# Kernel tuning notes

Hardware: AMD Instinct MI355X
Metric: run time of the kernel (lower is better)

Reference implementation:

```python
import jax, jax.numpy as jnp
import numpy as np

EPS = 1e-6
LOG2PI = float(np.log(2.0 * np.pi))


def gauss_lp(x, mu, lv):
    """Diagonal Gaussian log prob. x:[B,D], mu:[K,D], lv:[K,D] -> [B,K]."""
    inv_var = jnp.exp(-lv)                          # [K,D]
    d = x[:, None, :] - mu[None, :, :]              # [B,K,D]
    quad = jnp.sum(d * d * inv_var[None], axis=-1)  # [B,K]
    logdet = jnp.sum(lv, axis=-1)[None]             # [1,K]
    D = mu.shape[-1]
    return -0.5 * (quad + logdet + D * LOG2PI)


def setup_inputs() -> dict:
    key = jax.random.key(0)
    ks = jax.random.split(key, 9)
    T, B, S, A, OBS, CTL = 200, 256, 256, 16, 128, 16
    return {
        "x": jax.random.normal(ks[0], (T, B, OBS), jnp.float32),
        "u": jax.random.normal(ks[1], (T, B, CTL), jnp.float32),
        "obs_mu": jax.random.normal(ks[2], (S, OBS), jnp.float32),
        "obs_lv": 0.1 * jax.random.normal(ks[3], (S, OBS), jnp.float32),
        "ctl_mu": jax.random.normal(ks[4], (A, CTL), jnp.float32),
        "ctl_lv": 0.1 * jax.random.normal(ks[5], (A, CTL), jnp.float32),
        "trans_logits": jax.random.normal(ks[6], (A, S, S), jnp.float32),
        "pi0_logits": jax.random.normal(ks[7], (S,), jnp.float32),
        "act_prior": jax.random.normal(ks[8], (S, A), jnp.float32),
    }


def reference(x, u, obs_mu, obs_lv, ctl_mu, ctl_lv, trans_logits, pi0_logits, act_prior):
    """HMM forward algorithm (ContinuousGaussianHMM._forward).

    Returns:
      alpha_b: [T, B, S] state forward messages
      alpha_a: [T-1, B, A] action forward messages
    """
    S = obs_mu.shape[0]
    trans = jax.nn.softmax(trans_logits, axis=-1)      # [A,S,S]
    log_pi0 = jax.nn.log_softmax(pi0_logits)           # [S]

    # t = 0: initial state prior + observation likelihood
    b0 = jax.nn.softmax(gauss_lp(x[0], obs_mu, obs_lv) + log_pi0[None], axis=-1)  # [B,S]

    def step(b, xu):
        x_t, u_t = xu
        # action prior from belief: softmax(b @ act_prior)
        a_prior = jax.nn.softmax(b @ act_prior, axis=-1)                           # [B,A]
        # ctl_model.infer: posterior over actions given control u_t
        a_t = jax.nn.softmax(gauss_lp(u_t, ctl_mu, ctl_lv) + jnp.log(a_prior + EPS), axis=-1)  # [B,A]
        # action-conditioned transition applied to belief
        m = jnp.einsum('bi,kij->bkj', b, trans)                                    # [B,A,S]
        # original: sum_i(trans*b + eps) => einsum + S*eps
        logp_z = jnp.log(jnp.einsum('bk,bkj->bj', a_t, m) + S * EPS)               # [B,S]
        b_next = jax.nn.softmax(gauss_lp(x_t, obs_mu, obs_lv) + logp_z, axis=-1)   # [B,S]
        return b_next, (b_next, a_t)

    _, (bs, a_s) = jax.lax.scan(step, b0, (x[1:], u[:-1]))
    alpha_b = jnp.concatenate([b0[None], bs], axis=0)   # [T,B,S]
    alpha_a = a_s                                       # [T-1,B,A]
    return alpha_b, alpha_a
```

## Files before the change

kernel.cpp:

```cpp
#include <hip/hip_runtime.h>
#include <hip/hip_bf16.h>
#include <stdint.h>

#define T_STEPS 200
#define BATCH   256
#define NS      256
#define NA      16
#define DOBS    128
#define DCTL    16
#define LOG2PI  1.8378770664093453f
#define EPS_F   1e-6f

typedef float f32x4 __attribute__((ext_vector_type(4)));
typedef short s16x8 __attribute__((ext_vector_type(8)));
typedef short s16x4 __attribute__((ext_vector_type(4)));

static __device__ __forceinline__ unsigned short f2bf(float f) {
    union { float f; unsigned u; } v; v.f = f;
    unsigned u = v.u;
    u += 0x7fffu + ((u >> 16) & 1u);
    return (unsigned short)(u >> 16);
}

static __device__ __forceinline__ void ld4_mall(const float* base,
                                                f32x4& a, f32x4& b, f32x4& c, f32x4& d) {
    asm volatile(
        "global_load_dwordx4 %0, %4, off offset:0 sc0 sc1\n\t"
        "global_load_dwordx4 %1, %4, off offset:1024 sc0 sc1\n\t"
        "global_load_dwordx4 %2, %4, off offset:2048 sc0 sc1\n\t"
        "global_load_dwordx4 %3, %4, off offset:3072 sc0 sc1\n\t"
        "s_waitcnt vmcnt(0)"
        : "=&v"(a), "=&v"(b), "=&v"(c), "=&v"(d)
        : "v"(base)
        : "memory");
}
static __device__ __forceinline__ void st_mall(float* p, f32x4 v) {
    asm volatile("global_store_dwordx4 %0, %1, off sc0 sc1" :: "v"(p), "v"(v) : "memory");
}

__global__ __launch_bounds__(128) void k_prep_obs(const float* __restrict__ obs_mu,
                                                  const float* __restrict__ obs_lv,
                                                  float* __restrict__ WT,
                                                  float* __restrict__ Cs) {
    int s = blockIdx.x, d = threadIdx.x;
    float lv = obs_lv[s * DOBS + d];
    float mu = obs_mu[s * DOBS + d];
    float iv = expf(-lv);
    WT[d * NS + s]          = -0.5f * iv;
    WT[(DOBS + d) * NS + s] = mu * iv;
    float part = mu * mu * iv + lv;
    for (int m = 1; m < 64; m <<= 1) part += __shfl_xor(part, m, 64);
    __shared__ float red[2];
    if ((threadIdx.x & 63) == 0) red[threadIdx.x >> 6] = part;
    __syncthreads();
    if (threadIdx.x == 0) Cs[s] = -0.5f * (red[0] + red[1] + DOBS * LOG2PI);
}

__global__ __launch_bounds__(256) void k_prep_ctl(const float* __restrict__ cmu,
                                                  const float* __restrict__ clv,
                                                  float* __restrict__ cw1,
                                                  float* __restrict__ cw2,
                                                  float* __restrict__ cc) {
    int t = threadIdx.x;
    int a = t >> 4, d = t & 15;
    float lv = clv[a * DCTL + d];
    float mu = cmu[a * DCTL + d];
    float iv = expf(-lv);
    cw1[t] = -0.5f * iv;
    cw2[t] = mu * iv;
    float part = mu * mu * iv + lv;
    for (int m = 1; m < 16; m <<= 1) part += __shfl_xor(part, m, 64);
    if (d == 0) cc[a] = -0.5f * (part + DCTL * LOG2PI);
}

__global__ __launch_bounds__(64) void k_prep_pi0(const float* __restrict__ pl,
                                                 float* __restrict__ lpi0) {
    int l = threadIdx.x;
    float v[4]; float m = -1e30f;
    for (int k = 0; k < 4; k++) { v[k] = pl[l + 64 * k]; m = fmaxf(m, v[k]); }
    for (int mm = 1; mm < 64; mm <<= 1) m = fmaxf(m, __shfl_xor(m, mm, 64));
    float ssum = 0.f;
    for (int k = 0; k < 4; k++) ssum += expf(v[k] - m);
    for (int mm = 1; mm < 64; mm <<= 1) ssum += __shfl_xor(ssum, mm, 64);
    float ls = logf(ssum);
    for (int k = 0; k < 4; k++) lpi0[l + 64 * k] = v[k] - m - ls;
}

__global__ __launch_bounds__(256) void k_init(float* __restrict__ lg) {
    int idx = blockIdx.x * 256 + threadIdx.x;
    float nv = __int_as_float(0x7FC00000);
    f32x4 n4 = {nv, nv, nv, nv};
    st_mall(lg + (size_t)idx * 4, n4);
}

__global__ __launch_bounds__(256) void k_trans(const float* __restrict__ tl,
                                               __hip_bfloat16* __restrict__ TRf) {
    int wave = threadIdx.x >> 6, lane = threadIdx.x & 63;
    int row = blockIdx.x * 4 + wave;
    int a = row >> 8, i = row & 255;
    const float* src = tl + (size_t)row * NS;
    float v[4]; float m = -1e30f;
    for (int k = 0; k < 4; k++) { v[k] = src[lane + 64 * k]; m = fmaxf(m, v[k]); }
    for (int mm = 1; mm < 64; mm <<= 1) m = fmaxf(m, __shfl_xor(m, mm, 64));
    float ssum = 0.f; float ev[4];
    for (int k = 0; k < 4; k++) { ev[k] = expf(v[k] - m); ssum += ev[k]; }
    for (int mm = 1; mm < 64; mm <<= 1) ssum += __shfl_xor(ssum, mm, 64);
    float inv = 1.f / ssum;
    int kk = i >> 5;
    int lsub = ((i >> 3) & 3) * 16 + a;
    int e = i & 7;
    for (int k = 0; k < 4; k++) {
        int j = lane + 64 * k;
        float p = ev[k] * inv;
        TRf[((size_t)(j * 8 + kk) * 64 + lsub) * 8 + e] = __float2bfloat16(p);
    }
}

__global__ __launch_bounds__(64) void k_prep_ap(const float* __restrict__ ap,
                                                __hip_bfloat16* __restrict__ APh,
                                                __hip_bfloat16* __restrict__ APl) {
    int kk = blockIdx.x, lane = threadIdx.x;
    for (int e = 0; e < 8; e++) {
        int i = kk * 32 + (lane >> 4) * 8 + e;
        int a = lane & 15;
        float v = ap[i * NA + a];
        __hip_bfloat16 hb = __float2bfloat16(v);
        float hi = __bfloat162float(hb);
        APh[(kk * 64 + lane) * 8 + e] = hb;
        APl[(kk * 64 + lane) * 8 + e] = __float2bfloat16(v - hi);
    }
}

__global__ __launch_bounds__(256) void k_obslp(const float* __restrict__ x,
                                               const float* __restrict__ WT,
                                               const float* __restrict__ Cs,
                                               float* __restrict__ obs) {
    __shared__ float f[32 * 256];
    int r0 = blockIdx.x * 32;
    for (int idx = threadIdx.x; idx < 32 * DOBS; idx += 256) {
        int r = idx >> 7, d = idx & 127;
        float v = x[(size_t)(r0 + r) * DOBS + d];
        f[r * 256 + d] = v * v;
        f[r * 256 + 128 + d] = v;
    }
    __syncthreads();
    int s = threadIdx.x;
    float acc[32];
#pragma unroll
    for (int r = 0; r < 32; r++) acc[r] = 0.f;
    for (int d4 = 0; d4 < 64; d4++) {
        float w0 = WT[(d4 * 4 + 0) * NS + s];
        float w1 = WT[(d4 * 4 + 1) * NS + s];
        float w2 = WT[(d4 * 4 + 2) * NS + s];
        float w3 = WT[(d4 * 4 + 3) * NS + s];
#pragma unroll
        for (int r = 0; r < 32; r++) {
            f32x4 fv = *reinterpret_cast<const f32x4*>(&f[r * 256 + d4 * 4]);
            acc[r] += fv.x * w0 + fv.y * w1 + fv.z * w2 + fv.w * w3;
        }
    }
    float c = Cs[s];
#pragma unroll
    for (int r = 0; r < 32; r++) obs[(size_t)(r0 + r) * NS + s] = acc[r] + c;
}

__global__ __launch_bounds__(256) void k_ctllp(const float* __restrict__ u,
                                               const float* __restrict__ cw1,
                                               const float* __restrict__ cw2,
                                               const float* __restrict__ cc,
                                               float* __restrict__ ctl) {
    int idx = blockIdx.x * 256 + threadIdx.x;
    int r = idx >> 4, a = idx & 15;
    const float* ur = u + (size_t)r * DCTL;
    const float* w1 = cw1 + a * DCTL;
    const float* w2 = cw2 + a * DCTL;
    float acc = cc[a];
#pragma unroll
    for (int d = 0; d < 16; d++) {
        float uv = ur[d];
        acc += uv * uv * w1[d] + uv * w2[d];
    }
    ctl[idx] = acc;
}

struct ScanArgs {
    const float* obs;
    const float* ctlp;
    const float* lpi0;
    const __hip_bfloat16* TRf;
    const __hip_bfloat16* APh;
    const __hip_bfloat16* APl;
    float* lg;
    float* out_ab;
    float* out_aa;
};

__global__ __launch_bounds__(256, 1) void k_scan_p(ScanArgs A) {
    const int bid  = blockIdx.x;
    const int bt   = bid >> 4;
    const int jt   = bid & 15;
    const int tid  = threadIdx.x;
    const int wv   = tid >> 6, lane = tid & 63;
    const int kgrp = lane >> 4, arow = lane & 15;
    const int b0   = bt * 16;

    __shared__ __align__(16) char PLb[16 * 512];
    __shared__ float out_t[16][16];

    const float nv = __int_as_float(0x7FC00000);
    const f32x4 n4 = {nv, nv, nv, nv};

    s16x8 bfr[4][8];
#pragma unroll
    for (int q = 0; q < 4; q++) {
        int ct = jt * 16 + wv * 4 + q;
#pragma unroll
        for (int kk = 0; kk < 8; kk++)
            bfr[q][kk] = *((const s16x8*)A.TRf + (size_t)(ct * 8 + kk) * 64 + lane);
    }
    s16x8 aph[8], apl[8];
#pragma unroll
    for (int kk = 0; kk < 8; kk++) {
        aph[kk] = *((const s16x8*)A.APh + kk * 64 + lane);
        apl[kk] = *((const s16x8*)A.APl + kk * 64 + lane);
    }
    f32x4 lp0 = *(const f32x4*)&A.lpi0[lane * 4];

    const float* obs_pf_p = A.obs + ((size_t)BATCH + b0 + kgrp * 4) * NS + jt * 16 + wv * 4;
    const float* ctl_p    = A.ctlp + ((size_t)b0 + kgrp * 4) * NA + arow;
    float*       ab_p     = A.out_ab + ((size_t)b0 + wv * 4) * NS + lane * 4;
    float*       aa_p     = A.out_aa + ((size_t)b0 + kgrp * 4) * NA + arow;
    const float* obs0_p   = A.obs + (size_t)(b0 + wv * 4) * NS + lane * 4;
    const float* lg_ld    = A.lg + ((size_t)b0 + wv * 4) * NS + lane * 4;
    float*       lg_st    = A.lg + ((size_t)b0 + (lane >> 2)) * NS + jt * 16 + (lane & 3) * 4;

    for (int s = 0; s < T_STEPS - 1; s++) {
        f32x4 obs_pfv[4];
#pragma unroll
        for (int r = 0; r < 4; r++)
            obs_pfv[r] = *(const f32x4*)&obs_pf_p[r * NS];
        float ctl_pf[4];
#pragma unroll
        for (int q = 0; q < 4; q++)
            ctl_pf[q] = ctl_p[q * NA];

        f32x4 V[4];
        if (s == 0) {
#pragma unroll
            for (int q = 0; q < 4; q++) {
                f32x4 o = *(const f32x4*)&obs0_p[q * NS];
                V[q] = o + lp0;
            }
        } else {
            const float* rb = lg_ld + ((size_t)(s & 3) << 16);
            for (;;) {
                ld4_mall(rb, V[0], V[1], V[2], V[3]);
                float chk = ((V[0].x + V[0].y) + (V[0].z + V[0].w))
                          + ((V[1].x + V[1].y) + (V[1].z + V[1].w))
                          + ((V[2].x + V[2].y) + (V[2].z + V[2].w))
                          + ((V[3].x + V[3].y) + (V[3].z + V[3].w));
                if (chk == chk) break;
            }
        }

        if (s >= 2 && wv == 0)
            st_mall(lg_st + ((size_t)((s + 2) & 3) << 16), n4);

#pragma unroll
        for (int q = 0; q < 4; q++) {
            int r = wv * 4 + q;
            float m = fmaxf(fmaxf(V[q].x, V[q].y), fmaxf(V[q].z, V[q].w));
            for (int mm = 1; mm < 64; mm <<= 1) m = fmaxf(m, __shfl_xor(m, mm, 64));
            float e0 = __expf(V[q].x - m), e1 = __expf(V[q].y - m);
            float e2 = __expf(V[q].z - m), e3 = __expf(V[q].w - m);
            float ss = (e0 + e1) + (e2 + e3);
            for (int mm = 1; mm < 64; mm <<= 1) ss += __shfl_xor(ss, mm, 64);
            float inv = 1.f / ss;
            float p0 = e0 * inv, p1 = e1 * inv, p2 = e2 * inv, p3 = e3 * inv;
            if ((lane >> 2) == jt) {
                f32x4 pv = {p0, p1, p2, p3};
                *(f32x4*)&ab_p[q * NS] = pv;
            }
            s16x4 sv;
            sv[0] = (short)f2bf(p0); sv[1] = (short)f2bf(p1);
            sv[2] = (short)f2bf(p2); sv[3] = (short)f2bf(p3);
            *(s16x4*)(PLb + r * 512 + ((lane * 8) ^ ((r & 7) << 4))) = sv;
        }
        __syncthreads();

        s16x8 afr[8];
        {
            int sw = (arow & 7) << 4;
#pragma unroll
            for (int kk = 0; kk < 8; kk++)
                afr[kk] = *(const s16x8*)(PLb + arow * 512 + ((kk * 64 + kgrp * 16) ^ sw));
        }

        f32x4 gh = {0.f, 0.f, 0.f, 0.f}, gl = {0.f, 0.f, 0.f, 0.f};
#pragma unroll
        for (int kk = 0; kk < 8; kk++) {
            gh = __builtin_amdgcn_mfma_f32_16x16x32_bf16(afr[kk], aph[kk], gh, 0, 0, 0);
            gl = __builtin_amdgcn_mfma_f32_16x16x32_bf16(afr[kk], apl[kk], gl, 0, 0, 0);
        }
        float at[4];
#pragma unroll
        for (int q = 0; q < 4; q++) {
            float gv = gh[q] + gl[q];
            float m = gv;
            for (int mm = 1; mm < 16; mm <<= 1) m = fmaxf(m, __shfl_xor(m, mm, 64));
            float e1 = __expf(gv - m);
            float s1 = e1;
            for (int mm = 1; mm < 16; mm <<= 1) s1 += __shfl_xor(s1, mm, 64);
            float apr = e1 / s1;
            float al = ctl_pf[q] + __logf(apr + EPS_F);
            float m2 = al;
            for (int mm = 1; mm < 16; mm <<= 1) m2 = fmaxf(m2, __shfl_xor(m2, mm, 64));
            float e2 = __expf(al - m2);
            float s2 = e2;
            for (int mm = 1; mm < 16; mm <<= 1) s2 += __shfl_xor(s2, mm, 64);
            at[q] = e2 / s2;
            if (jt == 0)
                aa_p[q * NA] = at[q];
        }

#pragma unroll
        for (int q2 = 0; q2 < 4; q2++) {
            f32x4 acc = {0.f, 0.f, 0.f, 0.f};
#pragma unroll
            for (int kk = 0; kk < 8; kk++)
                acc = __builtin_amdgcn_mfma_f32_16x16x32_bf16(afr[kk], bfr[q2][kk], acc, 0, 0, 0);
#pragma unroll
            for (int r = 0; r < 4; r++) {
                float vv = acc[r] * at[r];
                for (int mm = 1; mm < 16; mm <<= 1) vv += __shfl_xor(vv, mm, 64);
                if (arow == 0)
                    out_t[kgrp * 4 + r][wv * 4 + q2] =
                        obs_pfv[r][q2] + __logf(vv + NS * EPS_F);
            }
        }
        __syncthreads();

        if (wv == 0) {
            f32x4 val = *(const f32x4*)&out_t[lane >> 2][(lane & 3) * 4];
            st_mall(lg_st + ((size_t)((s + 1) & 3) << 16), val);
        }
        obs_pf_p += (size_t)BATCH * NS;
        ctl_p    += (size_t)BATCH * NA;
        ab_p     += (size_t)BATCH * NS;
        aa_p     += (size_t)BATCH * NA;
    }

    f32x4 V[4];
    {
        const float* rb = lg_ld + ((size_t)((T_STEPS - 1) & 3) << 16);
        for (;;) {
            ld4_mall(rb, V[0], V[1], V[2], V[3]);
            float chk = ((V[0].x + V[0].y) + (V[0].z + V[0].w))
                      + ((V[1].x + V[1].y) + (V[1].z + V[1].w))
                      + ((V[2].x + V[2].y) + (V[2].z + V[2].w))
                      + ((V[3].x + V[3].y) + (V[3].z + V[3].w));
            if (chk == chk) break;
        }
    }
#pragma unroll
    for (int q = 0; q < 4; q++) {
        float m = fmaxf(fmaxf(V[q].x, V[q].y), fmaxf(V[q].z, V[q].w));
        for (int mm = 1; mm < 64; mm <<= 1) m = fmaxf(m, __shfl_xor(m, mm, 64));
        float e0 = __expf(V[q].x - m), e1 = __expf(V[q].y - m);
        float e2 = __expf(V[q].z - m), e3 = __expf(V[q].w - m);
        float ss = (e0 + e1) + (e2 + e3);
        for (int mm = 1; mm < 64; mm <<= 1) ss += __shfl_xor(ss, mm, 64);
        float inv = 1.f / ss;
        if ((lane >> 2) == jt) {
            f32x4 pv = {e0 * inv, e1 * inv, e2 * inv, e3 * inv};
            *(f32x4*)&ab_p[q * NS] = pv;
        }
    }
}

extern "C" void kernel_launch(void* const* d_in, const int* in_sizes, int n_in,
                              void* d_out, int out_size, void* d_ws, size_t ws_size,
                              hipStream_t stream) {
    const float* x            = (const float*)d_in[0];
    const float* u            = (const float*)d_in[1];
    const float* obs_mu       = (const float*)d_in[2];
    const float* obs_lv       = (const float*)d_in[3];
    const float* ctl_mu       = (const float*)d_in[4];
    const float* ctl_lv       = (const float*)d_in[5];
    const float* trans_logits = (const float*)d_in[6];
    const float* pi0_logits   = (const float*)d_in[7];
    const float* act_prior    = (const float*)d_in[8];

    float* out_ab = (float*)d_out;
    float* out_aa = out_ab + (size_t)T_STEPS * BATCH * NS;

    char* w = (char*)d_ws;
    size_t off = 0;
    auto alloc = [&](size_t bytes) -> void* {
        void* pp = w + off;
        off += (bytes + 255) & ~(size_t)255;
        return pp;
    };
    float* WT   = (float*)alloc((size_t)256 * 256 * 4);
    float* Cs   = (float*)alloc(256 * 4);
    float* cw1  = (float*)alloc(256 * 4);
    float* cw2  = (float*)alloc(256 * 4);
    float* cc   = (float*)alloc(16 * 4);
    float* lpi0 = (float*)alloc(256 * 4);
    __hip_bfloat16* TRf = (__hip_bfloat16*)alloc((size_t)4096 * 256 * 2);
    __hip_bfloat16* APh = (__hip_bfloat16*)alloc((size_t)8 * 64 * 8 * 2);
    __hip_bfloat16* APl = (__hip_bfloat16*)alloc((size_t)8 * 64 * 8 * 2);
    float* obs  = (float*)alloc((size_t)T_STEPS * BATCH * NS * 4);
    float* ctlp = (float*)alloc((size_t)(T_STEPS - 1) * BATCH * NA * 4);
    float* lg   = (float*)alloc((size_t)4 * BATCH * NS * 4);
    if (off > ws_size) return;

    k_init<<<256, 256, 0, stream>>>(lg);
    k_prep_obs<<<256, 128, 0, stream>>>(obs_mu, obs_lv, WT, Cs);
    k_prep_ctl<<<1, 256, 0, stream>>>(ctl_mu, ctl_lv, cw1, cw2, cc);
    k_prep_pi0<<<1, 64, 0, stream>>>(pi0_logits, lpi0);
    k_trans<<<1024, 256, 0, stream>>>(trans_logits, TRf);
    k_prep_ap<<<8, 64, 0, stream>>>(act_prior, APh, APl);
    k_obslp<<<1600, 256, 0, stream>>>(x, WT, Cs, obs);
    k_ctllp<<<3184, 256, 0, stream>>>(u, cw1, cw2, cc, ctlp);

    ScanArgs args;
    args.obs = obs; args.ctlp = ctlp; args.lpi0 = lpi0;
    args.TRf = TRf; args.APh = APh; args.APl = APl;
    args.lg = lg;
    args.out_ab = out_ab; args.out_aa = out_aa;
    k_scan_p<<<256, 256, 0, stream>>>(args);
}
```

Measured before the change: 2.087 ms.

## Fuse observation and control log-likelihood computation into the persistent scan kernel

Removes the separate k_obslp and k_ctllp precompute kernels and their large intermediate buffers. Each scan block now loads x and u per step, computes the Gaussian log-likelihoods for its 16 rows and 16 states/actions from weights staged in LDS, and uses them directly. This cuts the global write and read of the obs/ctl tensors and two launches. In exchange it adds per-step compute and an extra LDS pass on the sequential critical path. The step-0 initial belief is also computed in-kernel.

```diff
diff --git a/kernel.cpp b/kernel.cpp
--- a/kernel.cpp
+++ b/kernel.cpp
@@ -131,61 +131,14 @@
     }
 }
 
-__global__ __launch_bounds__(256) void k_obslp(const float* __restrict__ x,
-                                               const float* __restrict__ WT,
-                                               const float* __restrict__ Cs,
-                                               float* __restrict__ obs) {
-    __shared__ float f[32 * 256];
-    int r0 = blockIdx.x * 32;
-    for (int idx = threadIdx.x; idx < 32 * DOBS; idx += 256) {
-        int r = idx >> 7, d = idx & 127;
-        float v = x[(size_t)(r0 + r) * DOBS + d];
-        f[r * 256 + d] = v * v;
-        f[r * 256 + 128 + d] = v;
-    }
-    __syncthreads();
-    int s = threadIdx.x;
-    float acc[32];
-#pragma unroll
-    for (int r = 0; r < 32; r++) acc[r] = 0.f;
-    for (int d4 = 0; d4 < 64; d4++) {
-        float w0 = WT[(d4 * 4 + 0) * NS + s];
-        float w1 = WT[(d4 * 4 + 1) * NS + s];
-        float w2 = WT[(d4 * 4 + 2) * NS + s];
-        float w3 = WT[(d4 * 4 + 3) * NS + s];
-#pragma unroll
-        for (int r = 0; r < 32; r++) {
-            f32x4 fv = *reinterpret_cast<const f32x4*>(&f[r * 256 + d4 * 4]);
-            acc[r] += fv.x * w0 + fv.y * w1 + fv.z * w2 + fv.w * w3;
-        }
-    }
-    float c = Cs[s];
-#pragma unroll
-    for (int r = 0; r < 32; r++) obs[(size_t)(r0 + r) * NS + s] = acc[r] + c;
-}
-
-__global__ __launch_bounds__(256) void k_ctllp(const float* __restrict__ u,
-                                               const float* __restrict__ cw1,
-                                               const float* __restrict__ cw2,
-                                               const float* __restrict__ cc,
-                                               float* __restrict__ ctl) {
-    int idx = blockIdx.x * 256 + threadIdx.x;
-    int r = idx >> 4, a = idx & 15;
-    const float* ur = u + (size_t)r * DCTL;
-    const float* w1 = cw1 + a * DCTL;
-    const float* w2 = cw2 + a * DCTL;
-    float acc = cc[a];
-#pragma unroll
-    for (int d = 0; d < 16; d++) {
-        float uv = ur[d];
-        acc += uv * uv * w1[d] + uv * w2[d];
-    }
-    ctl[idx] = acc;
-}
-
 struct ScanArgs {
-    const float* obs;
-    const float* ctlp;
+    const float* x;
+    const float* u;
+    const float* WT;
+    const float* Cs;
+    const float* cw1;
+    const float* cw2;
+    const float* cc;
     const float* lpi0;
     const __hip_bfloat16* TRf;
     const __hip_bfloat16* APh;
@@ -203,9 +156,17 @@
     const int wv   = tid >> 6, lane = tid & 63;
     const int kgrp = lane >> 4, arow = lane & 15;
     const int b0   = bt * 16;
+    const int dr   = tid >> 4, dc = tid & 15;
 
     __shared__ __align__(16) char PLb[16 * 512];
     __shared__ float out_t[16][16];
+    __shared__ __align__(16) float fL[16][132];
+    __shared__ float uL[16][20];
+    __shared__ __align__(16) float W1L[16][132];
+    __shared__ __align__(16) float W2L[16][132];
+    __shared__ float cw1L[16][20], cw2L[16][20];
+    __shared__ float obsL[16][16];
+    __shared__ float ctlL[16][16];
 
     const float nv = __int_as_float(0x7FC00000);
     const f32x4 n4 = {nv, nv, nv, nv};
@@ -224,34 +185,85 @@
         aph[kk] = *((const s16x8*)A.APh + kk * 64 + lane);
         apl[kk] = *((const s16x8*)A.APl + kk * 64 + lane);
     }
-    f32x4 lp0 = *(const f32x4*)&A.lpi0[lane * 4];
-
-    const float* obs_pf_p = A.obs + ((size_t)BATCH + b0 + kgrp * 4) * NS + jt * 16 + wv * 4;
-    const float* ctl_p    = A.ctlp + ((size_t)b0 + kgrp * 4) * NA + arow;
-    float*       ab_p     = A.out_ab + ((size_t)b0 + wv * 4) * NS + lane * 4;
-    float*       aa_p     = A.out_aa + ((size_t)b0 + kgrp * 4) * NA + arow;
-    const float* obs0_p   = A.obs + (size_t)(b0 + wv * 4) * NS + lane * 4;
-    const float* lg_ld    = A.lg + ((size_t)b0 + wv * 4) * NS + lane * 4;
-    float*       lg_st    = A.lg + ((size_t)b0 + (lane >> 2)) * NS + jt * 16 + (lane & 3) * 4;
+
+    {
+        int dbase = dr * 8;
+#pragma unroll
+        for (int k = 0; k < 8; k++) {
+            W1L[dc][dbase + k] = A.WT[(size_t)(dbase + k) * NS + jt * 16 + dc];
+            W2L[dc][dbase + k] = A.WT[(size_t)(128 + dbase + k) * NS + jt * 16 + dc];
+        }
+        cw1L[dc][dr] = A.cw1[dc * DCTL + dr];
+        cw2L[dc][dr] = A.cw2[dc * DCTL + dr];
+    }
+    const float csv = A.Cs[jt * 16 + dc];
+    const float ccv = A.cc[dc];
+    const float lpv = A.lpi0[jt * 16 + dc];
+    __syncthreads();
+
+    float*       ab_p  = A.out_ab + ((size_t)b0 + wv * 4) * NS + lane * 4;
+    float*       aa_p  = A.out_aa + ((size_t)b0 + kgrp * 4) * NA + arow;
+    const float* lg_ld = A.lg + ((size_t)b0 + wv * 4) * NS + lane * 4;
+    float*       lg_st = A.lg + ((size_t)b0 + (lane >> 2)) * NS + jt * 16 + (lane & 3) * 4;
+    const float* x_p   = A.x + ((size_t)b0 + dr) * DOBS + dc * 8;
+    const float* u_p   = A.u + ((size_t)b0 + dr) * DCTL + dc;
+
+    {
+        f32x4 xa = *(const f32x4*)&x_p[0];
+        f32x4 xb = *(const f32x4*)&x_p[4];
+        *(f32x4*)&fL[dr][dc * 8]     = xa;
+        *(f32x4*)&fL[dr][dc * 8 + 4] = xb;
+        float acc = csv;
+#pragma unroll
+        for (int k = 0; k < 32; k++) {
+            f32x4 xv = *(const f32x4*)&fL[dr][k * 4];
+            f32x4 w1 = *(const f32x4*)&W1L[dc][k * 4];
+            f32x4 w2 = *(const f32x4*)&W2L[dc][k * 4];
+            acc += xv.x * xv.x * w1.x + xv.x * w2.x;
+            acc += xv.y * xv.y * w1.y + xv.y * w2.y;
+            acc += xv.z * xv.z * w1.z + xv.z * w2.z;
+            acc += xv.w * xv.w * w1.w + xv.w * w2.w;
+        }
+        out_t[dr][dc] = acc + lpv;
+        __syncthreads();
+        if (wv == 0) {
+            f32x4 val = *(const f32x4*)&out_t[lane >> 2][(lane & 3) * 4];
+            st_mall(lg_st, val);
+        }
+        x_p += (size_t)BATCH * DOBS;
+    }
 
     for (int s = 0; s < T_STEPS - 1; s++) {
-        f32x4 obs_pfv[4];
-#pragma unroll
-        for (int r = 0; r < 4; r++)
-            obs_pfv[r] = *(const f32x4*)&obs_pf_p[r * NS];
-        float ctl_pf[4];
-#pragma unroll
-        for (int q = 0; q < 4; q++)
-            ctl_pf[q] = ctl_p[q * NA];
+        {
+            f32x4 xa = *(const f32x4*)&x_p[0];
+            f32x4 xb = *(const f32x4*)&x_p[4];
+            float uv1 = u_p[0];
+            *(f32x4*)&fL[dr][dc * 8]     = xa;
+            *(f32x4*)&fL[dr][dc * 8 + 4] = xb;
+            uL[dr][dc] = uv1;
+            float acc = csv;
+#pragma unroll
+            for (int k = 0; k < 32; k++) {
+                f32x4 xv = *(const f32x4*)&fL[dr][k * 4];
+                f32x4 w1 = *(const f32x4*)&W1L[dc][k * 4];
+                f32x4 w2 = *(const f32x4*)&W2L[dc][k * 4];
+                acc += xv.x * xv.x * w1.x + xv.x * w2.x;
+                acc += xv.y * xv.y * w1.y + xv.y * w2.y;
+                acc += xv.z * xv.z * w1.z + xv.z * w2.z;
+                acc += xv.w * xv.w * w1.w + xv.w * w2.w;
+            }
+            obsL[dr][dc] = acc;
+            float ca = ccv;
+#pragma unroll
+            for (int d = 0; d < 16; d++) {
+                float uv = uL[dr][d];
+                ca += uv * uv * cw1L[dc][d] + uv * cw2L[dc][d];
+            }
+            ctlL[dr][dc] = ca;
+        }
 
         f32x4 V[4];
-        if (s == 0) {
-#pragma unroll
-            for (int q = 0; q < 4; q++) {
-                f32x4 o = *(const f32x4*)&obs0_p[q * NS];
-                V[q] = o + lp0;
-            }
-        } else {
+        {
             const float* rb = lg_ld + ((size_t)(s & 3) << 16);
             for (;;) {
                 ld4_mall(rb, V[0], V[1], V[2], V[3]);
@@ -312,7 +324,7 @@
             float s1 = e1;
             for (int mm = 1; mm < 16; mm <<= 1) s1 += __shfl_xor(s1, mm, 64);
             float apr = e1 / s1;
-            float al = ctl_pf[q] + __logf(apr + EPS_F);
+            float al = ctlL[kgrp * 4 + q][arow] + __logf(apr + EPS_F);
             float m2 = al;
             for (int mm = 1; mm < 16; mm <<= 1) m2 = fmaxf(m2, __shfl_xor(m2, mm, 64));
             float e2 = __expf(al - m2);
@@ -335,7 +347,7 @@
                 for (int mm = 1; mm < 16; mm <<= 1) vv += __shfl_xor(vv, mm, 64);
                 if (arow == 0)
                     out_t[kgrp * 4 + r][wv * 4 + q2] =
-                        obs_pfv[r][q2] + __logf(vv + NS * EPS_F);
+                        obsL[kgrp * 4 + r][wv * 4 + q2] + __logf(vv + NS * EPS_F);
             }
         }
         __syncthreads();
@@ -344,10 +356,10 @@
             f32x4 val = *(const f32x4*)&out_t[lane >> 2][(lane & 3) * 4];
             st_mall(lg_st + ((size_t)((s + 1) & 3) << 16), val);
         }
-        obs_pf_p += (size_t)BATCH * NS;
-        ctl_p    += (size_t)BATCH * NA;
-        ab_p     += (size_t)BATCH * NS;
-        aa_p     += (size_t)BATCH * NA;
+        x_p  += (size_t)BATCH * DOBS;
+        u_p  += (size_t)BATCH * DCTL;
+        ab_p += (size_t)BATCH * NS;
+        aa_p += (size_t)BATCH * NA;
     }
 
     f32x4 V[4];
@@ -410,8 +422,6 @@
     __hip_bfloat16* TRf = (__hip_bfloat16*)alloc((size_t)4096 * 256 * 2);
     __hip_bfloat16* APh = (__hip_bfloat16*)alloc((size_t)8 * 64 * 8 * 2);
     __hip_bfloat16* APl = (__hip_bfloat16*)alloc((size_t)8 * 64 * 8 * 2);
-    float* obs  = (float*)alloc((size_t)T_STEPS * BATCH * NS * 4);
-    float* ctlp = (float*)alloc((size_t)(T_STEPS - 1) * BATCH * NA * 4);
     float* lg   = (float*)alloc((size_t)4 * BATCH * NS * 4);
     if (off > ws_size) return;
 
@@ -421,11 +431,12 @@
     k_prep_pi0<<<1, 64, 0, stream>>>(pi0_logits, lpi0);
     k_trans<<<1024, 256, 0, stream>>>(trans_logits, TRf);
     k_prep_ap<<<8, 64, 0, stream>>>(act_prior, APh, APl);
-    k_obslp<<<1600, 256, 0, stream>>>(x, WT, Cs, obs);
-    k_ctllp<<<3184, 256, 0, stream>>>(u, cw1, cw2, cc, ctlp);
 
     ScanArgs args;
-    args.obs = obs; args.ctlp = ctlp; args.lpi0 = lpi0;
+    args.x = x; args.u = u;
+    args.WT = WT; args.Cs = Cs;
+    args.cw1 = cw1; args.cw2 = cw2; args.cc = cc;
+    args.lpi0 = lpi0;
     args.TRf = TRf; args.APh = APh; args.APl = APl;
     args.lg = lg;
     args.out_ab = out_ab; args.out_aa = out_aa;
```

Result: slower. 2.219 ms (+6.3%).

## Interleave two batch tiles per block to hide cross-block scan latency

Applied to the files above, without the earlier changes.

Each block now handles two batch tiles (bt and bt+8) and alternates their scan steps, with half as many blocks launched. While one tile waits on the cross-block exchange of log-messages through the global ring buffer, the block does useful work on the other tile, so the polling latency of the dependent recurrence is hidden. In exchange each block does twice the serial work per step and uses half the CUs, which adds compute time per step.

```diff
diff --git a/kernel.cpp b/kernel.cpp
--- a/kernel.cpp
+++ b/kernel.cpp
@@ -195,164 +195,143 @@
     float* out_aa;
 };
 
-__global__ __launch_bounds__(256, 1) void k_scan_p(ScanArgs A) {
-    const int bid  = blockIdx.x;
-    const int bt   = bid >> 4;
-    const int jt   = bid & 15;
-    const int tid  = threadIdx.x;
-    const int wv   = tid >> 6, lane = tid & 63;
-    const int kgrp = lane >> 4, arow = lane & 15;
-    const int b0   = bt * 16;
-
-    __shared__ __align__(16) char PLb[16 * 512];
-    __shared__ float out_t[16][16];
-
-    const float nv = __int_as_float(0x7FC00000);
-    const f32x4 n4 = {nv, nv, nv, nv};
-
-    s16x8 bfr[4][8];
+struct Ctx {
+    const float* obs_pf;
+    const float* ctl_p;
+    float*       ab_p;
+    float*       aa_p;
+    const float* obs0_p;
+    const float* lg_ld;
+    float*       lg_st;
+};
+
+static __device__ __forceinline__ void scan_phase(
+    int s, int jt, int lane, int wv, int kgrp, int arow, Ctx& C,
+    const s16x8 (&bfr)[4][8], const s16x8 (&aph)[8], const s16x8 (&apl)[8],
+    const f32x4& lp0, const f32x4& n4,
+    char* PLb, float (*out_t)[16])
+{
+    f32x4 obs_pfv[4];
+#pragma unroll
+    for (int r = 0; r < 4; r++)
+        obs_pfv[r] = *(const f32x4*)&C.obs_pf[r * NS];
+    float ctl_pf[4];
+#pragma unroll
+    for (int q = 0; q < 4; q++)
+        ctl_pf[q] = C.ctl_p[q * NA];
+
+    f32x4 V[4];
+    if (s == 0) {
+#pragma unroll
+        for (int q = 0; q < 4; q++) {
+            f32x4 o = *(const f32x4*)&C.obs0_p[q * NS];
+            V[q] = o + lp0;
+        }
+    } else {
+        const float* rb = C.lg_ld + ((size_t)(s & 3) << 16);
+        for (;;) {
+            ld4_mall(rb, V[0], V[1], V[2], V[3]);
+            float chk = ((V[0].x + V[0].y) + (V[0].z + V[0].w))
+                      + ((V[1].x + V[1].y) + (V[1].z + V[1].w))
+                      + ((V[2].x + V[2].y) + (V[2].z + V[2].w))
+                      + ((V[3].x + V[3].y) + (V[3].z + V[3].w));
+            if (chk == chk) break;
+        }
+    }
+
+    if (s >= 2 && wv == 0)
+        st_mall(C.lg_st + ((size_t)((s + 2) & 3) << 16), n4);
+
 #pragma unroll
     for (int q = 0; q < 4; q++) {
-        int ct = jt * 16 + wv * 4 + q;
+        int r = wv * 4 + q;
+        float m = fmaxf(fmaxf(V[q].x, V[q].y), fmaxf(V[q].z, V[q].w));
+        for (int mm = 1; mm < 64; mm <<= 1) m = fmaxf(m, __shfl_xor(m, mm, 64));
+        float e0 = __expf(V[q].x - m), e1 = __expf(V[q].y - m);
+        float e2 = __expf(V[q].z - m), e3 = __expf(V[q].w - m);
+        float ss = (e0 + e1) + (e2 + e3);
+        for (int mm = 1; mm < 64; mm <<= 1) ss += __shfl_xor(ss, mm, 64);
+        float inv = 1.f / ss;
+        float p0 = e0 * inv, p1 = e1 * inv, p2 = e2 * inv, p3 = e3 * inv;
+        if ((lane >> 2) == jt) {
+            f32x4 pv = {p0, p1, p2, p3};
+            *(f32x4*)&C.ab_p[q * NS] = pv;
+        }
+        s16x4 sv;
+        sv[0] = (short)f2bf(p0); sv[1] = (short)f2bf(p1);
+        sv[2] = (short)f2bf(p2); sv[3] = (short)f2bf(p3);
+        *(s16x4*)(PLb + r * 512 + ((lane * 8) ^ ((r & 7) << 4))) = sv;
+    }
+    __syncthreads();
+
+    s16x8 afr[8];
+    {
+        int sw = (arow & 7) << 4;
 #pragma unroll
         for (int kk = 0; kk < 8; kk++)
-            bfr[q][kk] = *((const s16x8*)A.TRf + (size_t)(ct * 8 + kk) * 64 + lane);
-    }
-    s16x8 aph[8], apl[8];
+            afr[kk] = *(const s16x8*)(PLb + arow * 512 + ((kk * 64 + kgrp * 16) ^ sw));
+    }
+
+    f32x4 gh = {0.f, 0.f, 0.f, 0.f}, gl = {0.f, 0.f, 0.f, 0.f};
 #pragma unroll
     for (int kk = 0; kk < 8; kk++) {
-        aph[kk] = *((const s16x8*)A.APh + kk * 64 + lane);
-        apl[kk] = *((const s16x8*)A.APl + kk * 64 + lane);
-    }
-    f32x4 lp0 = *(const f32x4*)&A.lpi0[lane * 4];
-
-    const float* obs_pf_p = A.obs + ((size_t)BATCH + b0 + kgrp * 4) * NS + jt * 16 + wv * 4;
-    const float* ctl_p    = A.ctlp + ((size_t)b0 + kgrp * 4) * NA + arow;
-    float*       ab_p     = A.out_ab + ((size_t)b0 + wv * 4) * NS + lane * 4;
-    float*       aa_p     = A.out_aa + ((size_t)b0 + kgrp * 4) * NA + arow;
-    const float* obs0_p   = A.obs + (size_t)(b0 + wv * 4) * NS + lane * 4;
-    const float* lg_ld    = A.lg + ((size_t)b0 + wv * 4) * NS + lane * 4;
-    float*       lg_st    = A.lg + ((size_t)b0 + (lane >> 2)) * NS + jt * 16 + (lane & 3) * 4;
-
-    for (int s = 0; s < T_STEPS - 1; s++) {
-        f32x4 obs_pfv[4];
-#pragma unroll
-        for (int r = 0; r < 4; r++)
-            obs_pfv[r] = *(const f32x4*)&obs_pf_p[r * NS];
-        float ctl_pf[4];
-#pragma unroll
-        for (int q = 0; q < 4; q++)
-            ctl_pf[q] = ctl_p[q * NA];
-
-        f32x4 V[4];
-        if (s == 0) {
-#pragma unroll
-            for (int q = 0; q < 4; q++) {
-                f32x4 o = *(const f32x4*)&obs0_p[q * NS];
-                V[q] = o + lp0;
-            }
-        } else {
-            const float* rb = lg_ld + ((size_t)(s & 3) << 16);
-            for (;;) {
-                ld4_mall(rb, V[0], V[1], V[2], V[3]);
-                float chk = ((V[0].x + V[0].y) + (V[0].z + V[0].w))
-                          + ((V[1].x + V[1].y) + (V[1].z + V[1].w))
-                          + ((V[2].x + V[2].y) + (V[2].z + V[2].w))
-                          + ((V[3].x + V[3].y) + (V[3].z + V[3].w));
-                if (chk == chk) break;
-            }
-        }
-
-        if (s >= 2 && wv == 0)
-            st_mall(lg_st + ((size_t)((s + 2) & 3) << 16), n4);
-
-#pragma unroll
-        for (int q = 0; q < 4; q++) {
-            int r = wv * 4 + q;
-            float m = fmaxf(fmaxf(V[q].x, V[q].y), fmaxf(V[q].z, V[q].w));
-            for (int mm = 1; mm < 64; mm <<= 1) m = fmaxf(m, __shfl_xor(m, mm, 64));
-            float e0 = __expf(V[q].x - m), e1 = __expf(V[q].y - m);
-            float e2 = __expf(V[q].z - m), e3 = __expf(V[q].w - m);
-            float ss = (e0 + e1) + (e2 + e3);
-            for (int mm = 1; mm < 64; mm <<= 1) ss += __shfl_xor(ss, mm, 64);
-            float inv = 1.f / ss;
-            float p0 = e0 * inv, p1 = e1 * inv, p2 = e2 * inv, p3 = e3 * inv;
-            if ((lane >> 2) == jt) {
-                f32x4 pv = {p0, p1, p2, p3};
-                *(f32x4*)&ab_p[q * NS] = pv;
-            }
-            s16x4 sv;
-            sv[0] = (short)f2bf(p0); sv[1] = (short)f2bf(p1);
-            sv[2] = (short)f2bf(p2); sv[3] = (short)f2bf(p3);
-            *(s16x4*)(PLb + r * 512 + ((lane * 8) ^ ((r & 7) << 4))) = sv;
-        }
-        __syncthreads();
-
-        s16x8 afr[8];
-        {
-            int sw = (arow & 7) << 4;
-#pragma unroll
-            for (int kk = 0; kk < 8; kk++)
-                afr[kk] = *(const s16x8*)(PLb + arow * 512 + ((kk * 64 + kgrp * 16) ^ sw));
-        }
-
-        f32x4 gh = {0.f, 0.f, 0.f, 0.f}, gl = {0.f, 0.f, 0.f, 0.f};
-#pragma unroll
-        for (int kk = 0; kk < 8; kk++) {
-            gh = __builtin_amdgcn_mfma_f32_16x16x32_bf16(afr[kk], aph[kk], gh, 0, 0, 0);
-            gl = __builtin_amdgcn_mfma_f32_16x16x32_bf16(afr[kk], apl[kk], gl, 0, 0, 0);
-        }
-        float at[4];
-#pragma unroll
-        for (int q = 0; q < 4; q++) {
-            float gv = gh[q] + gl[q];
-            float m = gv;
-            for (int mm = 1; mm < 16; mm <<= 1) m = fmaxf(m, __shfl_xor(m, mm, 64));
-            float e1 = __expf(gv - m);
-            float s1 = e1;
-            for (int mm = 1; mm < 16; mm <<= 1) s1 += __shfl_xor(s1, mm, 64);
-            float apr = e1 / s1;
-            float al = ctl_pf[q] + __logf(apr + EPS_F);
-            float m2 = al;
-            for (int mm = 1; mm < 16; mm <<= 1) m2 = fmaxf(m2, __shfl_xor(m2, mm, 64));
-            float e2 = __expf(al - m2);
-            float s2 = e2;
-            for (int mm = 1; mm < 16; mm <<= 1) s2 += __shfl_xor(s2, mm, 64);
-            at[q] = e2 / s2;
-            if (jt == 0)
-                aa_p[q * NA] = at[q];
-        }
-
-#pragma unroll
-        for (int q2 = 0; q2 < 4; q2++) {
-            f32x4 acc = {0.f, 0.f, 0.f, 0.f};
-#pragma unroll
-            for (int kk = 0; kk < 8; kk++)
-                acc = __builtin_amdgcn_mfma_f32_16x16x32_bf16(afr[kk], bfr[q2][kk], acc, 0, 0, 0);
-#pragma unroll
-            for (int r = 0; r < 4; r++) {
-                float vv = acc[r] * at[r];
-                for (int mm = 1; mm < 16; mm <<= 1) vv += __shfl_xor(vv, mm, 64);
-                if (arow == 0)
-                    out_t[kgrp * 4 + r][wv * 4 + q2] =
-                        obs_pfv[r][q2] + __logf(vv + NS * EPS_F);
-            }
-        }
-        __syncthreads();
-
-        if (wv == 0) {
-            f32x4 val = *(const f32x4*)&out_t[lane >> 2][(lane & 3) * 4];
-            st_mall(lg_st + ((size_t)((s + 1) & 3) << 16), val);
-        }
-        obs_pf_p += (size_t)BATCH * NS;
-        ctl_p    += (size_t)BATCH * NA;
-        ab_p     += (size_t)BATCH * NS;
-        aa_p     += (size_t)BATCH * NA;
-    }
-
+        gh = __builtin_amdgcn_mfma_f32_16x16x32_bf16(afr[kk], aph[kk], gh, 0, 0, 0);
+        gl = __builtin_amdgcn_mfma_f32_16x16x32_bf16(afr[kk], apl[kk], gl, 0, 0, 0);
+    }
+    float at[4];
+#pragma unroll
+    for (int q = 0; q < 4; q++) {
+        float gv = gh[q] + gl[q];
+        float m = gv;
+        for (int mm = 1; mm < 16; mm <<= 1) m = fmaxf(m, __shfl_xor(m, mm, 64));
+        float e1 = __expf(gv - m);
+        float s1 = e1;
+        for (int mm = 1; mm < 16; mm <<= 1) s1 += __shfl_xor(s1, mm, 64);
+        float apr = e1 / s1;
+        float al = ctl_pf[q] + __logf(apr + EPS_F);
+        float m2 = al;
+        for (int mm = 1; mm < 16; mm <<= 1) m2 = fmaxf(m2, __shfl_xor(m2, mm, 64));
+        float e2 = __expf(al - m2);
+        float s2 = e2;
+        for (int mm = 1; mm < 16; mm <<= 1) s2 += __shfl_xor(s2, mm, 64);
+        at[q] = e2 / s2;
+        if (jt == 0)
+            C.aa_p[q * NA] = at[q];
+    }
+
+#pragma unroll
+    for (int q2 = 0; q2 < 4; q2++) {
+        f32x4 acc = {0.f, 0.f, 0.f, 0.f};
+#pragma unroll
+        for (int kk = 0; kk < 8; kk++)
+            acc = __builtin_amdgcn_mfma_f32_16x16x32_bf16(afr[kk], bfr[q2][kk], acc, 0, 0, 0);
+#pragma unroll
+        for (int r = 0; r < 4; r++) {
+            float vv = acc[r] * at[r];
+            for (int mm = 1; mm < 16; mm <<= 1) vv += __shfl_xor(vv, mm, 64);
+            if (arow == 0)
+                out_t[kgrp * 4 + r][wv * 4 + q2] =
+                    obs_pfv[r][q2] + __logf(vv + NS * EPS_F);
+        }
+    }
+    __syncthreads();
+
+    if (wv == 0) {
+        f32x4 val = *(const f32x4*)&out_t[lane >> 2][(lane & 3) * 4];
+        st_mall(C.lg_st + ((size_t)((s + 1) & 3) << 16), val);
+    }
+    C.obs_pf += (size_t)BATCH * NS;
+    C.ctl_p  += (size_t)BATCH * NA;
+    C.ab_p   += (size_t)BATCH * NS;
+    C.aa_p   += (size_t)BATCH * NA;
+}
+
+static __device__ __forceinline__ void final_softmax(
+    int jt, int lane, const Ctx& C)
+{
     f32x4 V[4];
     {
-        const float* rb = lg_ld + ((size_t)((T_STEPS - 1) & 3) << 16);
+        const float* rb = C.lg_ld + ((size_t)((T_STEPS - 1) & 3) << 16);
         for (;;) {
             ld4_mall(rb, V[0], V[1], V[2], V[3]);
             float chk = ((V[0].x + V[0].y) + (V[0].z + V[0].w))
@@ -373,9 +352,64 @@
         float inv = 1.f / ss;
         if ((lane >> 2) == jt) {
             f32x4 pv = {e0 * inv, e1 * inv, e2 * inv, e3 * inv};
-            *(f32x4*)&ab_p[q * NS] = pv;
-        }
-    }
+            *(f32x4*)&C.ab_p[q * NS] = pv;
+        }
+    }
+}
+
+__global__ __launch_bounds__(256, 1) void k_scan_p(ScanArgs A) {
+    const int bid  = blockIdx.x;
+    const int btA  = bid >> 4;
+    const int btB  = btA + 8;
+    const int jt   = bid & 15;
+    const int tid  = threadIdx.x;
+    const int wv   = tid >> 6, lane = tid & 63;
+    const int kgrp = lane >> 4, arow = lane & 15;
+
+    __shared__ __align__(16) char PLb[16 * 512];
+    __shared__ float out_t[16][16];
+
+    const float nv = __int_as_float(0x7FC00000);
+    const f32x4 n4 = {nv, nv, nv, nv};
+
+    s16x8 bfr[4][8];
+#pragma unroll
+    for (int q = 0; q < 4; q++) {
+        int ct = jt * 16 + wv * 4 + q;
+#pragma unroll
+        for (int kk = 0; kk < 8; kk++)
+            bfr[q][kk] = *((const s16x8*)A.TRf + (size_t)(ct * 8 + kk) * 64 + lane);
+    }
+    s16x8 aph[8], apl[8];
+#pragma unroll
+    for (int kk = 0; kk < 8; kk++) {
+        aph[kk] = *((const s16x8*)A.APh + kk * 64 + lane);
+        apl[kk] = *((const s16x8*)A.APl + kk * 64 + lane);
+    }
+    f32x4 lp0 = *(const f32x4*)&A.lpi0[lane * 4];
+
+    auto mkctx = [&](int bt) -> Ctx {
+        int b0 = bt * 16;
+        Ctx C;
+        C.obs_pf = A.obs + ((size_t)BATCH + b0 + kgrp * 4) * NS + jt * 16 + wv * 4;
+        C.ctl_p  = A.ctlp + ((size_t)b0 + kgrp * 4) * NA + arow;
+        C.ab_p   = A.out_ab + ((size_t)b0 + wv * 4) * NS + lane * 4;
+        C.aa_p   = A.out_aa + ((size_t)b0 + kgrp * 4) * NA + arow;
+        C.obs0_p = A.obs + (size_t)(b0 + wv * 4) * NS + lane * 4;
+        C.lg_ld  = A.lg + ((size_t)b0 + wv * 4) * NS + lane * 4;
+        C.lg_st  = A.lg + ((size_t)b0 + (lane >> 2)) * NS + jt * 16 + (lane & 3) * 4;
+        return C;
+    };
+    Ctx CA = mkctx(btA);
+    Ctx CB = mkctx(btB);
+
+    for (int s = 0; s < T_STEPS - 1; s++) {
+        scan_phase(s, jt, lane, wv, kgrp, arow, CA, bfr, aph, apl, lp0, n4, PLb, out_t);
+        scan_phase(s, jt, lane, wv, kgrp, arow, CB, bfr, aph, apl, lp0, n4, PLb, out_t);
+    }
+
+    final_softmax(jt, lane, CA);
+    final_softmax(jt, lane, CB);
 }
 
 extern "C" void kernel_launch(void* const* d_in, const int* in_sizes, int n_in,
@@ -429,5 +463,5 @@
     args.TRf = TRf; args.APh = APh; args.APl = APl;
     args.lg = lg;
     args.out_ab = out_ab; args.out_aa = out_aa;
-    k_scan_p<<<256, 256, 0, stream>>>(args);
-}
+    k_scan_p<<<128, 256, 0, stream>>>(args);
+}
```

Measured after the change: 3.784 ms. 1.81x slower.

## Compute observation log-likelihoods with bf16 MFMA using hi/lo split precision

Applied to the files above, without the earlier changes.

Replaces the scalar FP32 dot-product kernel for observation log-probs with an MFMA kernel. Features (x^2, x) and weights are split into bf16 hi/lo pairs, and three MFMA products recover near-FP32 accuracy. A new prep kernel packs the weights into the MFMA operand layout, and LDS uses an XOR swizzle to avoid bank conflicts. This trades extra MFMA work and a small accuracy loss for moving the matmul off the vector ALUs.

```diff
diff --git a/kernel.cpp b/kernel.cpp
--- a/kernel.cpp
+++ b/kernel.cpp
@@ -20,6 +20,10 @@
     unsigned u = v.u;
     u += 0x7fffu + ((u >> 16) & 1u);
     return (unsigned short)(u >> 16);
+}
+static __device__ __forceinline__ float bf2f(unsigned short h) {
+    union { unsigned u; float f; } v; v.u = ((unsigned)h) << 16;
+    return v.f;
 }
 
 static __device__ __forceinline__ void ld4_mall(const float* base,
@@ -54,6 +58,22 @@
     if ((threadIdx.x & 63) == 0) red[threadIdx.x >> 6] = part;
     __syncthreads();
     if (threadIdx.x == 0) Cs[s] = -0.5f * (red[0] + red[1] + DOBS * LOG2PI);
+}
+
+__global__ __launch_bounds__(64) void k_prep_wf(const float* __restrict__ WT,
+                                                unsigned short* __restrict__ Wh,
+                                                unsigned short* __restrict__ Wl) {
+    int ct = blockIdx.x >> 3, kk = blockIdx.x & 7;
+    int lane = threadIdx.x;
+    for (int e = 0; e < 8; e++) {
+        int dp = kk * 32 + (lane >> 4) * 8 + e;
+        int s  = ct * 16 + (lane & 15);
+        float v = WT[(size_t)dp * NS + s];
+        unsigned short h = f2bf(v);
+        size_t idx = ((size_t)(ct * 8 + kk) * 64 + lane) * 8 + e;
+        Wh[idx] = h;
+        Wl[idx] = f2bf(v - bf2f(h));
+    }
 }
 
 __global__ __launch_bounds__(256) void k_prep_ctl(const float* __restrict__ cmu,
@@ -131,37 +151,79 @@
     }
 }
 
-__global__ __launch_bounds__(256) void k_obslp(const float* __restrict__ x,
-                                               const float* __restrict__ WT,
-                                               const float* __restrict__ Cs,
-                                               float* __restrict__ obs) {
-    __shared__ float f[32 * 256];
-    int r0 = blockIdx.x * 32;
-    for (int idx = threadIdx.x; idx < 32 * DOBS; idx += 256) {
-        int r = idx >> 7, d = idx & 127;
-        float v = x[(size_t)(r0 + r) * DOBS + d];
-        f[r * 256 + d] = v * v;
-        f[r * 256 + 128 + d] = v;
+__global__ __launch_bounds__(256) void k_obslp_mfma(const float* __restrict__ x,
+                                                    const unsigned short* __restrict__ Wh,
+                                                    const unsigned short* __restrict__ Wl,
+                                                    const float* __restrict__ Cs,
+                                                    float* __restrict__ obs) {
+    __shared__ __align__(16) char FhL[64 * 512];
+    __shared__ __align__(16) char FlL[64 * 512];
+    const int r0 = blockIdx.x * 64;
+    const int tid = threadIdx.x;
+
+    {
+        int row = tid >> 2, c0 = (tid & 3) * 32;
+        const float* xr = x + (size_t)(r0 + row) * DOBS + c0;
+        int sw = (row & 7) << 4;
+#pragma unroll
+        for (int g = 0; g < 8; g++) {
+            f32x4 v = *(const f32x4*)&xr[g * 4];
+            s16x4 sqh, sql, lih, lil;
+#pragma unroll
+            for (int e = 0; e < 4; e++) {
+                float sq = v[e] * v[e];
+                unsigned short h1 = f2bf(sq);
+                sqh[e] = (short)h1; sql[e] = (short)f2bf(sq - bf2f(h1));
+                unsigned short h2 = f2bf(v[e]);
+                lih[e] = (short)h2; lil[e] = (short)f2bf(v[e] - bf2f(h2));
+            }
+            int dp1 = (c0 + g * 4) * 2;
+            int dp2 = (128 + c0 + g * 4) * 2;
+            *(s16x4*)(FhL + row * 512 + (dp1 ^ sw)) = sqh;
+            *(s16x4*)(FlL + row * 512 + (dp1 ^ sw)) = sql;
+            *(s16x4*)(FhL + row * 512 + (dp2 ^ sw)) = lih;
+            *(s16x4*)(FlL + row * 512 + (dp2 ^ sw)) = lil;
+        }
     }
     __syncthreads();
-    int s = threadIdx.x;
-    float acc[32];
-#pragma unroll
-    for (int r = 0; r < 32; r++) acc[r] = 0.f;
-    for (int d4 = 0; d4 < 64; d4++) {
-        float w0 = WT[(d4 * 4 + 0) * NS + s];
-        float w1 = WT[(d4 * 4 + 1) * NS + s];
-        float w2 = WT[(d4 * 4 + 2) * NS + s];
-        float w3 = WT[(d4 * 4 + 3) * NS + s];
-#pragma unroll
-        for (int r = 0; r < 32; r++) {
-            f32x4 fv = *reinterpret_cast<const f32x4*>(&f[r * 256 + d4 * 4]);
-            acc[r] += fv.x * w0 + fv.y * w1 + fv.z * w2 + fv.w * w3;
-        }
-    }
-    float c = Cs[s];
-#pragma unroll
-    for (int r = 0; r < 32; r++) obs[(size_t)(r0 + r) * NS + s] = acc[r] + c;
+
+    const int wv = tid >> 6, lane = tid & 63;
+    const int kgrp = lane >> 4, arow = lane & 15;
+
+    for (int rt = 0; rt < 4; rt++) {
+        int rr = rt * 16 + arow;
+        int sw = (rr & 7) << 4;
+        s16x8 ah[8], al[8];
+#pragma unroll
+        for (int kk = 0; kk < 8; kk++) {
+            ah[kk] = *(const s16x8*)(FhL + rr * 512 + ((kk * 64 + kgrp * 16) ^ sw));
+            al[kk] = *(const s16x8*)(FlL + rr * 512 + ((kk * 64 + kgrp * 16) ^ sw));
+        }
+        f32x4 acc[4];
+#pragma unroll
+        for (int ci = 0; ci < 4; ci++) acc[ci] = (f32x4){0.f, 0.f, 0.f, 0.f};
+#pragma unroll
+        for (int ci = 0; ci < 4; ci++) {
+            int ct = wv * 4 + ci;
+#pragma unroll
+            for (int kk = 0; kk < 8; kk++) {
+                s16x8 bh = *((const s16x8*)Wh + (size_t)(ct * 8 + kk) * 64 + lane);
+                s16x8 bl = *((const s16x8*)Wl + (size_t)(ct * 8 + kk) * 64 + lane);
+                acc[ci] = __builtin_amdgcn_mfma_f32_16x16x32_bf16(ah[kk], bh, acc[ci], 0, 0, 0);
+                acc[ci] = __builtin_amdgcn_mfma_f32_16x16x32_bf16(ah[kk], bl, acc[ci], 0, 0, 0);
+                acc[ci] = __builtin_amdgcn_mfma_f32_16x16x32_bf16(al[kk], bh, acc[ci], 0, 0, 0);
+            }
+        }
+#pragma unroll
+        for (int ci = 0; ci < 4; ci++) {
+            int ct = wv * 4 + ci;
+            float cv = Cs[ct * 16 + arow];
+#pragma unroll
+            for (int r = 0; r < 4; r++)
+                obs[(size_t)(r0 + rt * 16 + kgrp * 4 + r) * NS + ct * 16 + arow] =
+                    acc[ci][r] + cv;
+        }
+    }
 }
 
 __global__ __launch_bounds__(256) void k_ctllp(const float* __restrict__ u,
@@ -410,6 +472,8 @@
     __hip_bfloat16* TRf = (__hip_bfloat16*)alloc((size_t)4096 * 256 * 2);
     __hip_bfloat16* APh = (__hip_bfloat16*)alloc((size_t)8 * 64 * 8 * 2);
     __hip_bfloat16* APl = (__hip_bfloat16*)alloc((size_t)8 * 64 * 8 * 2);
+    unsigned short* Wh  = (unsigned short*)alloc((size_t)16 * 8 * 64 * 8 * 2);
+    unsigned short* Wl  = (unsigned short*)alloc((size_t)16 * 8 * 64 * 8 * 2);
     float* obs  = (float*)alloc((size_t)T_STEPS * BATCH * NS * 4);
     float* ctlp = (float*)alloc((size_t)(T_STEPS - 1) * BATCH * NA * 4);
     float* lg   = (float*)alloc((size_t)4 * BATCH * NS * 4);
@@ -417,11 +481,12 @@
 
     k_init<<<256, 256, 0, stream>>>(lg);
     k_prep_obs<<<256, 128, 0, stream>>>(obs_mu, obs_lv, WT, Cs);
+    k_prep_wf<<<128, 64, 0, stream>>>(WT, Wh, Wl);
     k_prep_ctl<<<1, 256, 0, stream>>>(ctl_mu, ctl_lv, cw1, cw2, cc);
     k_prep_pi0<<<1, 64, 0, stream>>>(pi0_logits, lpi0);
     k_trans<<<1024, 256, 0, stream>>>(trans_logits, TRf);
     k_prep_ap<<<8, 64, 0, stream>>>(act_prior, APh, APl);
-    k_obslp<<<1600, 256, 0, stream>>>(x, WT, Cs, obs);
+    k_obslp_mfma<<<800, 256, 0, stream>>>(x, Wh, Wl, Cs, obs);
     k_ctllp<<<3184, 256, 0, stream>>>(u, cw1, cw2, cc, ctlp);
 
     ScanArgs args;
```

Result: faster. 1.956 ms (-6.3%).
